# Kernel tuning notes

Measured on AMD Instinct MI355X. Metric: run time of the kernel, lower is better.

## Reference

```python
import jax, jax.numpy as jnp
import numpy as np

N, E, F, H, T, K = 50000, 800000, 128, 128, 10, 3


def setup_inputs() -> dict:
    key = jax.random.key(0)
    ks = jax.random.split(key, 12)
    def p(k, shape):
        return jax.random.normal(k, shape, dtype=jnp.float32) * 0.05
    inp = {
        "x": jax.random.normal(ks[0], (N, F), dtype=jnp.float32),
        "edge_index": jax.random.randint(ks[1], (2, E), 0, N, dtype=jnp.int64),
        "edge_weight": jax.random.uniform(ks[2], (E,), dtype=jnp.float32),
    }
    names = ["xz", "hz", "xr", "hr", "xh", "hh"]
    for i, nm in enumerate(names):
        cin = F if nm[0] == "x" else H
        inp["W" + nm] = p(ks[3 + i], (K, cin, H))  # ChebConv: K linear maps [in,out]
        inp["b" + nm] = jnp.zeros((H,), jnp.float32)
    inp["Wlin"] = p(ks[9], (H, T))
    inp["blin"] = jnp.zeros((T,), jnp.float32)
    return inp


def _cheb_norm(src, dst, edge_weight, n):
    # PyG ChebConv norm with normalization='sym', lambda_max=2.0:
    # L_hat = 2L/lambda_max - I = -D^{-1/2} A D^{-1/2}  (zero diagonal)
    deg = jax.ops.segment_sum(edge_weight, src, num_segments=n)
    deg_safe = jnp.where(deg > 0, deg, 1.0)
    dinv = jnp.where(deg > 0, jax.lax.rsqrt(deg_safe), 0.0)
    return -dinv[src] * edge_weight * dinv[dst]


def _cheb_conv(x, W, b, src, dst, norm, n):
    # out = sum_k T_k(L_hat) x @ W[k] + b, via Chebyshev recurrence
    def prop(t):  # L_hat @ t : gather from source nodes, scatter-add into targets
        return jax.ops.segment_sum(norm[:, None] * t[src], dst, num_segments=n)
    Tx0 = x
    out = Tx0 @ W[0]
    Tx1 = prop(Tx0)
    out = out + Tx1 @ W[1]
    for k in range(2, W.shape[0]):
        Tx2 = 2.0 * prop(Tx1) - Tx0
        out = out + Tx2 @ W[k]
        Tx0, Tx1 = Tx1, Tx2
    return out + b


def reference(x, edge_index, edge_weight, Wxz, bxz, Whz, bhz, Wxr, bxr,
              Whr, bhr, Wxh, bxh, Whh, bhh, Wlin, blin):
    n = x.shape[0]
    src, dst = edge_index[0], edge_index[1]
    norm = _cheb_norm(src, dst, edge_weight, n)
    Hs = jnp.zeros((n, Whz.shape[2]), x.dtype)  # GConvGRU inits H=None -> zeros
    Z = jax.nn.sigmoid(_cheb_conv(x, Wxz, bxz, src, dst, norm, n)
                       + _cheb_conv(Hs, Whz, bhz, src, dst, norm, n))
    R = jax.nn.sigmoid(_cheb_conv(x, Wxr, bxr, src, dst, norm, n)
                       + _cheb_conv(Hs, Whr, bhr, src, dst, norm, n))
    Ht = jnp.tanh(_cheb_conv(x, Wxh, bxh, src, dst, norm, n)
                  + _cheb_conv(Hs * R, Whh, bhh, src, dst, norm, n))
    Hn = Z * Hs + (1.0 - Z) * Ht
    return Hn @ Wlin + blin
```

## Files before the change

kernel.cpp:

```cpp
#include <hip/hip_runtime.h>
#include <hip/hip_fp16.h>

typedef __attribute__((ext_vector_type(8))) short bf16x8;
typedef __attribute__((ext_vector_type(4))) float f32x4;
typedef unsigned int u32;
typedef unsigned short u16;

#define CAP 48

static __device__ __forceinline__ u16 f2bf(float f) {
  u32 u = __float_as_uint(f);
  u32 r = (u + 0x7fffu + ((u >> 16) & 1u)) >> 16;
  return (u16)r;
}
static __device__ __forceinline__ u32 f2h15(float f) {
  __half h = __float2half(f);
  return (u32)(((__half_raw)h).x) & 0x7FFFu;
}
static __device__ __forceinline__ float h152f(u32 b) {
  __half_raw hr; hr.x = (u16)b;
  return __half2float(__half(hr));
}
static __device__ __forceinline__ void gload16(const void* g, void* l) {
  __builtin_amdgcn_global_load_lds((const __attribute__((address_space(1))) u32*)g,
                                   (__attribute__((address_space(3))) u32*)l, 16, 0, 0);
}

__global__ __launch_bounds__(256) void mega_kernel(
    const float* __restrict__ x, const int* __restrict__ ei, const float* __restrict__ w,
    const float* __restrict__ Wxz, const float* __restrict__ Wxh,
    const float* __restrict__ bxz, const float* __restrict__ bhz,
    const float* __restrict__ bxh, const float* __restrict__ bhh,
    u32* __restrict__ xw, float* __restrict__ deg, int* __restrict__ cur,
    u32* __restrict__ edges, u16* __restrict__ Bp, float* __restrict__ bzs,
    float* __restrict__ bhs, int E, int N, int nw, int eb, int pbBase, int interleave) {
  int bid = blockIdx.x, tid = threadIdx.x;
  if (bid >= pbBase) {
    int idx = (bid - pbBase) * 256 + tid;
    int j = idx & 7, h4 = (idx >> 3) & 3, n = (idx >> 5) & 15, ct = (idx >> 9) & 15, kt = idx >> 13;
    int k = kt * 32 + h4 * 8 + j;
    int c = ct * 16 + n;
    int kb = k >> 7, ci = k & 127, h = c >> 1;
    const float* W = (c & 1) ? Wxh : Wxz;
    float v = W[((size_t)kb * 128 + ci) * 128 + h];
    Bp[idx] = f2bf(v);
    if (idx < 128) { bzs[idx] = bxz[idx] + bhz[idx]; bhs[idx] = bxh[idx] + bhh[idx]; }
    return;
  }
  int role, g;
  if (interleave) { int r = bid % 6; g = bid / 6; role = (r >= 2) ? 2 : r; if (r >= 2) g = g * 4 + (r - 2); }
  else { if (bid < eb) { role = 0; g = bid; } else if (bid < 2 * eb) { role = 1; g = bid - eb; } else { role = 2; g = bid - 2 * eb; } }

  if (role == 2) {
    int i = g * 256 + tid;
    if (i < nw) {
      float2 v = *(const float2*)&x[(size_t)i * 2];
      xw[i] = (u32)f2bf(v.x) | ((u32)f2bf(v.y) << 16);
    }
  } else if (role == 0) {
    int e = g * 256 + tid;
    if (e < E) {
      int s = ei[e];
      if ((unsigned)s < (unsigned)N) atomicAdd(&deg[s], w[e]);
    }
  } else {
    int e = g * 256 + tid;
    if (e < E) {
      int s = ei[e], d = ei[E + e];
      if ((unsigned)s < (unsigned)N && (unsigned)d < (unsigned)N) {
        u32 rec = ((u32)s << 15) | f2h15(w[e]);
        int pos = atomicAdd(&cur[d], 1);
        if (pos < CAP) edges[d * CAP + pos] = rec;
      }
    }
  }
}

#define ACC16(VV, NN)                                                   \
  _Pragma("unroll") for (int k_ = 0; k_ < 16; ++k_) {                   \
    a0 += NN[k_] * __uint_as_float(VV[k_] << 16);                       \
    a1 += NN[k_] * __uint_as_float(VV[k_] & 0xffff0000u);               \
  }

__global__ __launch_bounds__(256) void prop1_kernel(const u32* __restrict__ xw,
    const float* __restrict__ deg, const u32* __restrict__ edges, const int* __restrict__ cur,
    u32* __restrict__ t1w, int N) {
  int node = (blockIdx.x << 2) + (threadIdx.x >> 6);
  if (node >= N) return;
  int lane = threadIdx.x & 63;
  int len = cur[node]; if (len > CAP) len = CAP;
  u32 rec = edges[node * CAP + (lane < CAP ? lane : CAP - 1)];
  u32 sbase = (rec >> 15) << 6;
  float dgs = (lane < len) ? deg[rec >> 15] : 1.f;
  float nvl = (lane < len && dgs > 0.f) ? h152f(rec & 0x7FFFu) * rsqrtf(dgs) : 0.f;
  float a0 = 0.f, a1 = 0.f;
  u32 v[16]; float nv[16];
#pragma unroll
  for (int k = 0; k < 16; ++k) {
    u32 sb = (u32)__shfl((int)sbase, k);
    float n = __shfl(nvl, k);
    if (k < len) { v[k] = xw[sb | (unsigned)lane]; nv[k] = n; }
    else { v[k] = 0; nv[k] = 0.f; }
  }
  for (int base = 0; base < len; base += 16) {
    u32 vv[16]; float nn[16];
#pragma unroll
    for (int k = 0; k < 16; ++k) { vv[k] = v[k]; nn[k] = nv[k]; }
#pragma unroll
    for (int k = 0; k < 16; ++k) {
      int kn = base + 16 + k;
      u32 sb = (u32)__shfl((int)sbase, kn);
      float n = __shfl(nvl, kn);
      if (kn < len) { v[k] = xw[sb | (unsigned)lane]; nv[k] = n; }
      else { v[k] = 0; nv[k] = 0.f; }
    }
    ACC16(vv, nn);
  }
  float dd = deg[node];
  float di = dd > 0.f ? -rsqrtf(dd) : 0.f;
  unsigned idx = ((unsigned)node << 6) | (unsigned)lane;
  t1w[idx] = (u32)f2bf(di * a0) | ((u32)f2bf(di * a1) << 16);
}

__global__ __launch_bounds__(256) void prop2_kernel(const u32* __restrict__ xw,
    const u32* __restrict__ t1w, const float* __restrict__ deg,
    const u32* __restrict__ edges, const int* __restrict__ cur,
    u32* __restrict__ t2w, int N) {
  int node = (blockIdx.x << 2) + (threadIdx.x >> 6);
  if (node >= N) return;
  int lane = threadIdx.x & 63;
  int len = cur[node]; if (len > CAP) len = CAP;
  u32 rec = edges[node * CAP + (lane < CAP ? lane : CAP - 1)];
  u32 sbase = (rec >> 15) << 6;
  float dgs = (lane < len) ? deg[rec >> 15] : 1.f;
  float nvl = (lane < len && dgs > 0.f) ? h152f(rec & 0x7FFFu) * rsqrtf(dgs) : 0.f;
  float a0 = 0.f, a1 = 0.f;
  u32 v[16]; float nv[16];
#pragma unroll
  for (int k = 0; k < 16; ++k) {
    u32 sb = (u32)__shfl((int)sbase, k);
    float n = __shfl(nvl, k);
    if (k < len) { v[k] = t1w[sb | (unsigned)lane]; nv[k] = n; }
    else { v[k] = 0; nv[k] = 0.f; }
  }
  for (int base = 0; base < len; base += 16) {
    u32 vv[16]; float nn[16];
#pragma unroll
    for (int k = 0; k < 16; ++k) { vv[k] = v[k]; nn[k] = nv[k]; }
#pragma unroll
    for (int k = 0; k < 16; ++k) {
      int kn = base + 16 + k;
      u32 sb = (u32)__shfl((int)sbase, kn);
      float n = __shfl(nvl, kn);
      if (kn < len) { v[k] = t1w[sb | (unsigned)lane]; nv[k] = n; }
      else { v[k] = 0; nv[k] = 0.f; }
    }
    ACC16(vv, nn);
  }
  float dd = deg[node];
  float di = dd > 0.f ? rsqrtf(dd) : 0.f;
  unsigned idx = ((unsigned)node << 6) | (unsigned)lane;
  u32 xv = xw[idx];
  float r0 = -2.f * di * a0 - __uint_as_float(xv << 16);
  float r1 = -2.f * di * a1 - __uint_as_float(xv & 0xffff0000u);
  t2w[idx] = (u32)f2bf(r0) | ((u32)f2bf(r1) << 16);
}

__global__ __launch_bounds__(512, 2) void gemm_kernel(
    const u16* __restrict__ xb, const u16* __restrict__ t1, const u16* __restrict__ t2,
    const u16* __restrict__ Bp, const float* __restrict__ bzs, const float* __restrict__ bhs,
    const float* __restrict__ Wlin, const float* __restrict__ blin,
    float* __restrict__ out, int N) {
  __shared__ __align__(16) char smem[49152];
  const int offB_[2] = {0, 16384};
  const int offA_[2] = {32768, 40960};

  int tid = threadIdx.x;
  int w = tid >> 6, lane = tid & 63;
  int l15 = lane & 15, lh = lane >> 4;
  int rowBase = blockIdx.x << 7;
  int wrow = (w >> 2) << 6;
  int wcol = (w & 3) << 6;

  const u16* acts[3] = {xb, t1, t2};

  f32x4 acc[4][4];
  f32x4 zero = {0.f, 0.f, 0.f, 0.f};
#pragma unroll
  for (int mi = 0; mi < 4; ++mi)
#pragma unroll
    for (int ni = 0; ni < 4; ++ni) acc[mi][ni] = zero;

  auto stageB = [&](int kt, int buf) {
    const char* g = (const char*)Bp + kt * 16384 + w * 2048 + lane * 16;
    char* l = smem + offB_[buf] + w * 2048;
    gload16(g, l);
    gload16(g + 1024, l + 1024);
  };
  auto stageA = [&](int kt, int buf) {
    int kb = kt >> 2;
    const u16* act = acts[kb];
    int rl = (w << 4) + (lane >> 2);
    int grow = rowBase + rl; if (grow >= N) grow = N - 1;
    int hsw = (lane & 3) ^ ((rl >> 1) & 3);
    const char* g = (const char*)act + (size_t)grow * 256 + ((kt & 3) << 6) + (hsw << 4);
    char* l = smem + offA_[buf] + (w << 10);
    gload16(g, l);
  };

  stageB(0, 0); stageA(0, 0);

#pragma unroll
  for (int kt = 0; kt < 12; ++kt) {
    __syncthreads();
    if (kt < 11) { stageB(kt + 1, (kt + 1) & 1); stageA(kt + 1, (kt + 1) & 1); }
    const char* Ab = smem + offA_[kt & 1];
    const char* Bb = smem + offB_[kt & 1];
    bf16x8 a[4], b[4];
#pragma unroll
    for (int mi = 0; mi < 4; ++mi) {
      int row = wrow + (mi << 4) + l15;
      int off = (row << 6) + ((lh ^ ((row >> 1) & 3)) << 4);
      a[mi] = *(const bf16x8*)(Ab + off);
    }
#pragma unroll
    for (int ni = 0; ni < 4; ++ni) {
      int ct = ((w & 3) << 2) + ni;
      int off = (((ct << 4) + l15) << 6) + (lh << 4);
      b[ni] = *(const bf16x8*)(Bb + off);
    }
#pragma unroll
    for (int mi = 0; mi < 4; ++mi)
#pragma unroll
      for (int ni = 0; ni < 4; ++ni)
        acc[mi][ni] = __builtin_amdgcn_mfma_f32_16x16x32_bf16(a[mi], b[ni], acc[mi][ni], 0, 0, 0);
  }

  __syncthreads();

  u16* HnS = (u16*)smem;
  float* WlS = (float*)(smem + 34816);
  float* blS = (float*)(smem + 34816 + 5120);
  for (int i = tid; i < 1280; i += 512) WlS[i] = Wlin[i];
  if (tid < 10) blS[tid] = blin[tid];

  int odd = lane & 1;
#pragma unroll
  for (int ni = 0; ni < 4; ++ni) {
    int h = (wcol + (ni << 4) + l15) >> 1;
    float badd = odd ? bhs[h] : bzs[h];
#pragma unroll
    for (int mi = 0; mi < 4; ++mi)
#pragma unroll
      for (int reg = 0; reg < 4; ++reg) {
        float pre = acc[mi][ni][reg] + badd;
        float s2 = odd ? 2.f * pre : pre;
        float e = __expf(s2);
        float A = odd ? 1.f : 0.f;
        float B = odd ? 2.f : -1.f;
        float r = A - B / (1.f + e);
        float o = __shfl_xor(r, 1);
        if (!odd) {
          int row = wrow + (mi << 4) + (lh << 2) + reg;
          HnS[row * 136 + h] = f2bf(r * o);
        }
      }
  }
  __syncthreads();

  for (int idx = tid; idx < 1280; idx += 512) {
    int row = idx / 10, t = idx - row * 10;
    int grow = rowBase + row;
    if (grow < N) {
      float s = blS[t];
      const u16* hr = HnS + row * 136;
#pragma unroll 4
      for (int hc = 0; hc < 16; ++hc) {
        uint4 q = *(const uint4*)(hr + (hc << 3));
        const float* wp = WlS + (hc << 3) * 10 + t;
        s += __uint_as_float(q.x << 16) * wp[0];
        s += __uint_as_float(q.x & 0xffff0000u) * wp[10];
        s += __uint_as_float(q.y << 16) * wp[20];
        s += __uint_as_float(q.y & 0xffff0000u) * wp[30];
        s += __uint_as_float(q.z << 16) * wp[40];
        s += __uint_as_float(q.z & 0xffff0000u) * wp[50];
        s += __uint_as_float(q.w << 16) * wp[60];
        s += __uint_as_float(q.w & 0xffff0000u) * wp[70];
      }
      out[(size_t)grow * 10 + t] = s;
    }
  }
}

extern "C" void kernel_launch(void* const* d_in, const int* in_sizes, int n_in,
                              void* d_out, int out_size, void* d_ws, size_t ws_size,
                              hipStream_t stream) {
  const float* x    = (const float*)d_in[0];
  const int*   ei   = (const int*)d_in[1];
  const float* w    = (const float*)d_in[2];
  const float* Wxz  = (const float*)d_in[3];
  const float* bxz  = (const float*)d_in[4];
  const float* bhz  = (const float*)d_in[6];
  const float* Wxh  = (const float*)d_in[11];
  const float* bxh  = (const float*)d_in[12];
  const float* bhh  = (const float*)d_in[14];
  const float* Wlin = (const float*)d_in[15];
  const float* blin = (const float*)d_in[16];
  float* out = (float*)d_out;

  int N = in_sizes[0] / 128;
  int E = in_sizes[2];

  char* p = (char*)d_ws;
  auto alloc = [&](size_t bytes) {
    char* r = p;
    p += (bytes + 255) & ~(size_t)255;
    return r;
  };
  float* deg   = (float*)alloc((size_t)N * 8);
  int*   cur   = (int*)(deg + N);
  u32*   edges = (u32*)alloc((size_t)N * CAP * 4);
  u32*   xbw   = (u32*)alloc((size_t)N * 256);
  u32*   t1w   = (u32*)alloc((size_t)N * 256);
  u32*   t2w   = (u32*)alloc((size_t)N * 256);
  u16*   Bp    = (u16*)alloc(196608);
  float* bzs   = (float*)alloc(512);
  float* bhs   = (float*)alloc(512);

  hipMemsetAsync(deg, 0, (size_t)N * 8, stream);

  int nw = N * 64;
  int eb = (E + 255) / 256;
  int cb = (nw + 255) / 256;
  int interleave = (cb == 4 * eb) ? 1 : 0;
  int workB = interleave ? 6 * eb : (2 * eb + cb);
  int pbBase = workB;
  int grid = workB + 384;

  hipLaunchKernelGGL(mega_kernel, dim3(grid), dim3(256), 0, stream,
                     x, ei, w, Wxz, Wxh, bxz, bhz, bxh, bhh,
                     xbw, deg, cur, edges, Bp, bzs, bhs, E, N, nw, eb, pbBase, interleave);
  int nb = (N + 3) / 4;
  hipLaunchKernelGGL(prop1_kernel, dim3(nb), dim3(256), 0, stream, xbw, deg, edges, cur, t1w, N);
  hipLaunchKernelGGL(prop2_kernel, dim3(nb), dim3(256), 0, stream, xbw, t1w, deg, edges, cur, t2w, N);
  int gb = (N + 127) / 128;
  hipLaunchKernelGGL(gemm_kernel, dim3(gb), dim3(512), 0, stream,
                     (const u16*)xbw, (const u16*)t1w, (const u16*)t2w, Bp, bzs, bhs,
                     Wlin, blin, out, N);
}
```

Before: 302.6 us.

## Gather neighbor rows with 16-byte loads, four edges per wavefront in parallel

The propagation kernels now split each 64-lane wavefront into four 16-lane quarters. Each quarter handles a different neighbor edge, and each lane loads a uint4 (8 bf16 features), replacing one 32-bit word per lane per edge. Partial sums are reduced across the quarters with xor shuffles, and a single quarter writes the result with vector stores. The aim is fewer, wider memory instructions and more edges in flight per wavefront. The cost is extra shuffle reductions, more accumulator registers, and idle lanes at the store.

```diff
diff --git a/kernel.cpp b/kernel.cpp
--- a/kernel.cpp
+++ b/kernel.cpp
@@ -76,94 +76,95 @@
   }
 }
 
-#define ACC16(VV, NN)                                                   \
-  _Pragma("unroll") for (int k_ = 0; k_ < 16; ++k_) {                   \
-    a0 += NN[k_] * __uint_as_float(VV[k_] << 16);                       \
-    a1 += NN[k_] * __uint_as_float(VV[k_] & 0xffff0000u);               \
+#define PROP_BODY(SRCARR)                                                            \
+  int node = (blockIdx.x << 2) + (threadIdx.x >> 6);                                 \
+  if (node >= N) return;                                                             \
+  int lane = threadIdx.x & 63;                                                       \
+  int q = lane >> 4, fl = lane & 15;                                                 \
+  int len = cur[node]; if (len > CAP) len = CAP;                                     \
+  u32 rec = edges[node * CAP + (lane < CAP ? lane : CAP - 1)];                       \
+  u32 sbase = (rec >> 15) << 6;                                                      \
+  float dgs = (lane < len) ? deg[rec >> 15] : 1.f;                                   \
+  float nvl = (lane < len && dgs > 0.f) ? h152f(rec & 0x7FFFu) * rsqrtf(dgs) : 0.f;  \
+  float a[8];                                                                        \
+  _Pragma("unroll") for (int f = 0; f < 8; ++f) a[f] = 0.f;                          \
+  uint4 v[4]; float nv4[4];                                                          \
+  int iters = (len + 3) >> 2;                                                        \
+  _Pragma("unroll") for (int i = 0; i < 4; ++i) {                                    \
+    int j = 4 * i + q;                                                               \
+    u32 sb = (u32)__shfl((int)sbase, j);                                             \
+    float n = __shfl(nvl, j);                                                        \
+    if (j < len) { v[i] = *(const uint4*)&SRCARR[sb + (fl << 2)]; nv4[i] = n; }      \
+    else { v[i] = make_uint4(0, 0, 0, 0); nv4[i] = 0.f; }                            \
+  }                                                                                  \
+  for (int base = 0; base < iters; base += 4) {                                      \
+    uint4 vv[4]; float nn[4];                                                        \
+    _Pragma("unroll") for (int k = 0; k < 4; ++k) { vv[k] = v[k]; nn[k] = nv4[k]; }  \
+    _Pragma("unroll") for (int k = 0; k < 4; ++k) {                                  \
+      int j = 4 * (base + 4 + k) + q;                                                \
+      u32 sb = (u32)__shfl((int)sbase, j & 63);                                      \
+      float n = __shfl(nvl, j & 63);                                                 \
+      if (j < len) { v[k] = *(const uint4*)&SRCARR[sb + (fl << 2)]; nv4[k] = n; }    \
+      else { v[k] = make_uint4(0, 0, 0, 0); nv4[k] = 0.f; }                          \
+    }                                                                                \
+    _Pragma("unroll") for (int k = 0; k < 4; ++k) {                                  \
+      float n = nn[k];                                                               \
+      a[0] += n * __uint_as_float(vv[k].x << 16);                                    \
+      a[1] += n * __uint_as_float(vv[k].x & 0xffff0000u);                            \
+      a[2] += n * __uint_as_float(vv[k].y << 16);                                    \
+      a[3] += n * __uint_as_float(vv[k].y & 0xffff0000u);                            \
+      a[4] += n * __uint_as_float(vv[k].z << 16);                                    \
+      a[5] += n * __uint_as_float(vv[k].z & 0xffff0000u);                            \
+      a[6] += n * __uint_as_float(vv[k].w << 16);                                    \
+      a[7] += n * __uint_as_float(vv[k].w & 0xffff0000u);                            \
+    }                                                                                \
+  }                                                                                  \
+  _Pragma("unroll") for (int f = 0; f < 8; ++f) {                                    \
+    a[f] += __shfl_xor(a[f], 16);                                                    \
+    a[f] += __shfl_xor(a[f], 32);                                                    \
   }
 
 __global__ __launch_bounds__(256) void prop1_kernel(const u32* __restrict__ xw,
     const float* __restrict__ deg, const u32* __restrict__ edges, const int* __restrict__ cur,
     u32* __restrict__ t1w, int N) {
-  int node = (blockIdx.x << 2) + (threadIdx.x >> 6);
-  if (node >= N) return;
-  int lane = threadIdx.x & 63;
-  int len = cur[node]; if (len > CAP) len = CAP;
-  u32 rec = edges[node * CAP + (lane < CAP ? lane : CAP - 1)];
-  u32 sbase = (rec >> 15) << 6;
-  float dgs = (lane < len) ? deg[rec >> 15] : 1.f;
-  float nvl = (lane < len && dgs > 0.f) ? h152f(rec & 0x7FFFu) * rsqrtf(dgs) : 0.f;
-  float a0 = 0.f, a1 = 0.f;
-  u32 v[16]; float nv[16];
-#pragma unroll
-  for (int k = 0; k < 16; ++k) {
-    u32 sb = (u32)__shfl((int)sbase, k);
-    float n = __shfl(nvl, k);
-    if (k < len) { v[k] = xw[sb | (unsigned)lane]; nv[k] = n; }
-    else { v[k] = 0; nv[k] = 0.f; }
-  }
-  for (int base = 0; base < len; base += 16) {
-    u32 vv[16]; float nn[16];
-#pragma unroll
-    for (int k = 0; k < 16; ++k) { vv[k] = v[k]; nn[k] = nv[k]; }
-#pragma unroll
-    for (int k = 0; k < 16; ++k) {
-      int kn = base + 16 + k;
-      u32 sb = (u32)__shfl((int)sbase, kn);
-      float n = __shfl(nvl, kn);
-      if (kn < len) { v[k] = xw[sb | (unsigned)lane]; nv[k] = n; }
-      else { v[k] = 0; nv[k] = 0.f; }
-    }
-    ACC16(vv, nn);
-  }
-  float dd = deg[node];
-  float di = dd > 0.f ? -rsqrtf(dd) : 0.f;
-  unsigned idx = ((unsigned)node << 6) | (unsigned)lane;
-  t1w[idx] = (u32)f2bf(di * a0) | ((u32)f2bf(di * a1) << 16);
+  PROP_BODY(xw)
+  if (q == 0) {
+    float dd = deg[node];
+    float di = dd > 0.f ? -rsqrtf(dd) : 0.f;
+    uint4 o;
+    o.x = (u32)f2bf(di * a[0]) | ((u32)f2bf(di * a[1]) << 16);
+    o.y = (u32)f2bf(di * a[2]) | ((u32)f2bf(di * a[3]) << 16);
+    o.z = (u32)f2bf(di * a[4]) | ((u32)f2bf(di * a[5]) << 16);
+    o.w = (u32)f2bf(di * a[6]) | ((u32)f2bf(di * a[7]) << 16);
+    *(uint4*)&t1w[((unsigned)node << 6) | (unsigned)(fl << 2)] = o;
+  }
 }
 
 __global__ __launch_bounds__(256) void prop2_kernel(const u32* __restrict__ xw,
     const u32* __restrict__ t1w, const float* __restrict__ deg,
     const u32* __restrict__ edges, const int* __restrict__ cur,
     u32* __restrict__ t2w, int N) {
-  int node = (blockIdx.x << 2) + (threadIdx.x >> 6);
-  if (node >= N) return;
-  int lane = threadIdx.x & 63;
-  int len = cur[node]; if (len > CAP) len = CAP;
-  u32 rec = edges[node * CAP + (lane < CAP ? lane : CAP - 1)];
-  u32 sbase = (rec >> 15) << 6;
-  float dgs = (lane < len) ? deg[rec >> 15] : 1.f;
-  float nvl = (lane < len && dgs > 0.f) ? h152f(rec & 0x7FFFu) * rsqrtf(dgs) : 0.f;
-  float a0 = 0.f, a1 = 0.f;
-  u32 v[16]; float nv[16];
-#pragma unroll
-  for (int k = 0; k < 16; ++k) {
-    u32 sb = (u32)__shfl((int)sbase, k);
-    float n = __shfl(nvl, k);
-    if (k < len) { v[k] = t1w[sb | (unsigned)lane]; nv[k] = n; }
-    else { v[k] = 0; nv[k] = 0.f; }
-  }
-  for (int base = 0; base < len; base += 16) {
-    u32 vv[16]; float nn[16];
-#pragma unroll
-    for (int k = 0; k < 16; ++k) { vv[k] = v[k]; nn[k] = nv[k]; }
-#pragma unroll
-    for (int k = 0; k < 16; ++k) {
-      int kn = base + 16 + k;
-      u32 sb = (u32)__shfl((int)sbase, kn);
-      float n = __shfl(nvl, kn);
-      if (kn < len) { v[k] = t1w[sb | (unsigned)lane]; nv[k] = n; }
-      else { v[k] = 0; nv[k] = 0.f; }
-    }
-    ACC16(vv, nn);
-  }
-  float dd = deg[node];
-  float di = dd > 0.f ? rsqrtf(dd) : 0.f;
-  unsigned idx = ((unsigned)node << 6) | (unsigned)lane;
-  u32 xv = xw[idx];
-  float r0 = -2.f * di * a0 - __uint_as_float(xv << 16);
-  float r1 = -2.f * di * a1 - __uint_as_float(xv & 0xffff0000u);
-  t2w[idx] = (u32)f2bf(r0) | ((u32)f2bf(r1) << 16);
+  PROP_BODY(t1w)
+  if (q == 0) {
+    float dd = deg[node];
+    float di = dd > 0.f ? rsqrtf(dd) : 0.f;
+    uint4 xv = *(const uint4*)&xw[((unsigned)node << 6) | (unsigned)(fl << 2)];
+    uint4 o;
+    float r0, r1;
+    r0 = -2.f * di * a[0] - __uint_as_float(xv.x << 16);
+    r1 = -2.f * di * a[1] - __uint_as_float(xv.x & 0xffff0000u);
+    o.x = (u32)f2bf(r0) | ((u32)f2bf(r1) << 16);
+    r0 = -2.f * di * a[2] - __uint_as_float(xv.y << 16);
+    r1 = -2.f * di * a[3] - __uint_as_float(xv.y & 0xffff0000u);
+    o.y = (u32)f2bf(r0) | ((u32)f2bf(r1) << 16);
+    r0 = -2.f * di * a[4] - __uint_as_float(xv.z << 16);
+    r1 = -2.f * di * a[5] - __uint_as_float(xv.z & 0xffff0000u);
+    o.z = (u32)f2bf(r0) | ((u32)f2bf(r1) << 16);
+    r0 = -2.f * di * a[6] - __uint_as_float(xv.w << 16);
+    r1 = -2.f * di * a[7] - __uint_as_float(xv.w & 0xffff0000u);
+    o.w = (u32)f2bf(r0) | ((u32)f2bf(r1) << 16);
+    *(uint4*)&t2w[((unsigned)node << 6) | (unsigned)(fl << 2)] = o;
+  }
 }
 
 __global__ __launch_bounds__(512, 2) void gemm_kernel(
```

Measured after the change: 288.1 us. 4.8% less time.
